# Performance work log

Measured on AMD Instinct MI355X. Metric: run time of the kernel, lower is better.

## Reference

```python
import jax, jax.numpy as jnp
import numpy as np

N_NODES = 50000


def _gcn_norm(edge_index, num_nodes):
    # Add self-loops (PyG GCNConv default, fill_value=1.0) and compute
    # symmetric normalization: norm_e = d^-1/2[row_e] * d^-1/2[col_e].
    loops = jnp.arange(num_nodes, dtype=edge_index.dtype)
    row = jnp.concatenate([edge_index[0], loops])
    col = jnp.concatenate([edge_index[1], loops])
    w = jnp.ones(row.shape[0], dtype=jnp.float32)
    deg = jax.ops.segment_sum(w, col, num_segments=num_nodes)
    dinv = jnp.where(deg > 0, jax.lax.rsqrt(deg), 0.0)
    norm = dinv[row] * w * dinv[col]
    return row, col, norm


def _gcn_conv(x, W, b, row, col, norm, num_nodes):
    h = x @ W                               # [N, out] dense GEMM
    msg = h[row] * norm[:, None]            # gather + scale  [E2, out]
    out = jax.ops.segment_sum(msg, col, num_segments=num_nodes)
    return out + b


def setup_inputs() -> dict:
    key = jax.random.key(0)
    k1, k2, k3, k4 = jax.random.split(key, 4)
    F, H, C, E = 512, 256, 64, 800000
    x = jax.random.normal(k1, (N_NODES, F), dtype=jnp.float32)
    edge_index = jax.random.randint(k2, (2, E), 0, N_NODES, dtype=jnp.int64)
    W1 = jax.random.normal(k3, (F, H), dtype=jnp.float32) * (1.0 / np.sqrt(F))
    b1 = jnp.zeros((H,), dtype=jnp.float32)
    W2 = jax.random.normal(k4, (H, C), dtype=jnp.float32) * (1.0 / np.sqrt(H))
    b2 = jnp.zeros((C,), dtype=jnp.float32)
    return {"x": x, "edge_index": edge_index, "W1": W1, "b1": b1, "W2": W2, "b2": b2}


def reference(x, edge_index, W1, b1, W2, b2):
    n = x.shape[0]
    row, col, norm = _gcn_norm(edge_index, n)
    h = _gcn_conv(x, W1, b1, row, col, norm, n)
    h = jax.nn.relu(h)                      # dropout is identity in eval
    out = _gcn_conv(h, W2, b2, row, col, norm, n)
    return out                              # do_omit_softmax=False -> Identity head
```

## Files before the change

kernel.cpp:

```cpp
#include <hip/hip_runtime.h>


typedef __bf16 bf16x8 __attribute__((ext_vector_type(8)));
typedef __bf16 bf16x4 __attribute__((ext_vector_type(4)));
typedef float  f32x4  __attribute__((ext_vector_type(4)));

#define N_NODES  50000
#define N_PAD    50048
#define ZERO_ROW 50000
#define F_IN     512
#define F_HID    256
#define F_OUT    64
#define SCAN_B   196

__global__ __launch_bounds__(256) void convw_kernel(
    const float* __restrict__ W, __bf16* __restrict__ WT, int K, int N)
{
    int i = blockIdx.x * blockDim.x + threadIdx.x;
    if (i >= N * K) return;
    int n = i / K, k = i - n * K;
    WT[i] = (__bf16)W[(size_t)k * N + n];
}

__global__ __launch_bounds__(256) void initsrc_kernel(
    int* __restrict__ srcidx, int n4)
{
    int i = blockIdx.x * blockDim.x + threadIdx.x;
    if (i < n4) {
        int4 v = make_int4(ZERO_ROW, ZERO_ROW, ZERO_ROW, ZERO_ROW);
        *(int4*)(srcidx + i * 4) = v;
    }
}

__global__ __launch_bounds__(256) void count_kernel(
    const int* __restrict__ col, int E, int Nn, int* __restrict__ cnt)
{
    int e0 = (blockIdx.x * blockDim.x + threadIdx.x) * 4;
    if (e0 >= E) return;
    int4 cc = *(const int4*)(col + e0);
    if ((unsigned)cc.x < (unsigned)Nn) atomicAdd(&cnt[cc.x], 1);
    if ((unsigned)cc.y < (unsigned)Nn) atomicAdd(&cnt[cc.y], 1);
    if ((unsigned)cc.z < (unsigned)Nn) atomicAdd(&cnt[cc.z], 1);
    if ((unsigned)cc.w < (unsigned)Nn) atomicAdd(&cnt[cc.w], 1);
}

__global__ __launch_bounds__(256) void scan_partial_kernel(
    const int* __restrict__ cnt, int* __restrict__ bsum, int N)
{
    __shared__ int s[256];
    const int t = threadIdx.x;
    const int i = blockIdx.x * 256 + t;
    int v = (i < N) ? ((cnt[i] + 1 + 7) & ~7) : 0;
    s[t] = v;
    __syncthreads();
    #pragma unroll
    for (int off = 128; off > 0; off >>= 1) {
        if (t < off) s[t] += s[t + off];
        __syncthreads();
    }
    if (t == 0) bsum[blockIdx.x] = s[0];
}

__global__ __launch_bounds__(256) void scan_bsum_kernel(
    const int* __restrict__ bsum, int* __restrict__ bofs,
    int* __restrict__ offs, int N, int PB)
{
    __shared__ int s[256];
    const int t = threadIdx.x;
    int v = (t < PB) ? bsum[t] : 0;
    s[t] = v;
    __syncthreads();
    #pragma unroll
    for (int off = 1; off < 256; off <<= 1) {
        int u = (t >= off) ? s[t - off] : 0;
        __syncthreads();
        s[t] += u;
        __syncthreads();
    }
    if (t < PB) bofs[t] = s[t] - v;
    if (t == 255) offs[N] = s[255];
}

__global__ __launch_bounds__(256) void scan_fill_kernel(
    const int* __restrict__ cnt, const int* __restrict__ bofs,
    int* __restrict__ offs, float* __restrict__ dinv, int N)
{
    __shared__ int s[256];
    const int t = threadIdx.x;
    const int i = blockIdx.x * 256 + t;
    int c   = (i < N) ? cnt[i] + 1 : 0;
    int cap = (c + 7) & ~7;
    s[t] = cap;
    __syncthreads();
    #pragma unroll
    for (int off = 1; off < 256; off <<= 1) {
        int u = (t >= off) ? s[t - off] : 0;
        __syncthreads();
        s[t] += u;
        __syncthreads();
    }
    if (i < N) {
        offs[i] = bofs[blockIdx.x] + s[t] - cap;
        dinv[i] = rsqrtf((float)c);
    }
}

__global__ __launch_bounds__(256) void fill_kernel(
    const int* __restrict__ row, const int* __restrict__ col,
    int E, int Nn, const int* __restrict__ offs,
    int* __restrict__ fill, int* __restrict__ srcidx)
{
    int e0 = (blockIdx.x * blockDim.x + threadIdx.x) * 4;
    int total = E + Nn;
    if (e0 >= total) return;
    int rr[4], cc[4];
    #pragma unroll
    for (int j = 0; j < 4; ++j) {
        int e = e0 + j;
        if (e < E)      { cc[j] = col[e]; rr[j] = row[e]; }
        else            { int i = e - E; cc[j] = (i < Nn) ? i : -1; rr[j] = cc[j]; }
    }
    #pragma unroll
    for (int j = 0; j < 4; ++j) {
        int c = cc[j], r = rr[j];
        if ((unsigned)c < (unsigned)Nn && (unsigned)r < (unsigned)Nn) {
            int p = offs[c] + atomicAdd(&fill[c], 1);
            srcidx[p] = r;
        }
    }
}

__global__ __launch_bounds__(256, 2) void gemm1_kernel(
    const float* __restrict__ A, const __bf16* __restrict__ BT,
    const float* __restrict__ dinv, __bf16* __restrict__ C)
{
    const int tid  = threadIdx.x;
    const int lane = tid & 63;
    const int wid  = tid >> 6;
    const int wm = wid >> 1, wn = wid & 1;
    const int bm = blockIdx.x * 64;
    const int lr = lane & 15, kg = lane >> 4;

    const int row0 = bm + wm * 32 + lr;
    const int row1 = row0 + 16;
    const int r0c = (row0 < N_NODES) ? row0 : 0;
    const int r1c = (row1 < N_NODES) ? row1 : 0;
    const float*  pa0 = A  + (size_t)r0c * F_IN + kg * 8;
    const float*  pa1 = A  + (size_t)r1c * F_IN + kg * 8;
    const __bf16* pb  = BT + (size_t)(wn * 128 + lr) * F_IN + kg * 8;

    float4 fa[4][2][2];
    bf16x8 fb[2][8];
    f32x4  acc[2][8] = {};

#define LA(i) {                                                    \
        fa[(i) & 3][0][0] = *(const float4*)(pa0 + (i) * 32);      \
        fa[(i) & 3][0][1] = *(const float4*)(pa0 + (i) * 32 + 4);  \
        fa[(i) & 3][1][0] = *(const float4*)(pa1 + (i) * 32);      \
        fa[(i) & 3][1][1] = *(const float4*)(pa1 + (i) * 32 + 4); }
#define LB(i) {                                                    \
        _Pragma("unroll")                                          \
        for (int n = 0; n < 8; ++n)                                \
            fb[(i) & 1][n] = *(const bf16x8*)(pb + (size_t)n * 16 * F_IN + (i) * 32); }

    LA(0) LA(1) LA(2)
    LB(0)

    #pragma unroll
    for (int kc = 0; kc < 16; ++kc) {
        if (kc + 3 < 16) LA(kc + 3)
        if (kc + 1 < 16) LB(kc + 1)
        bf16x8 wa[2];
        #pragma unroll
        for (int m = 0; m < 2; ++m) {
            float4 x0 = fa[kc & 3][m][0], x1 = fa[kc & 3][m][1];
            wa[m][0]=(__bf16)x0.x; wa[m][1]=(__bf16)x0.y;
            wa[m][2]=(__bf16)x0.z; wa[m][3]=(__bf16)x0.w;
            wa[m][4]=(__bf16)x1.x; wa[m][5]=(__bf16)x1.y;
            wa[m][6]=(__bf16)x1.z; wa[m][7]=(__bf16)x1.w;
        }
        #pragma unroll
        for (int m = 0; m < 2; ++m)
            #pragma unroll
            for (int n = 0; n < 8; ++n)
                acc[m][n] = __builtin_amdgcn_mfma_f32_16x16x32_bf16(
                    wa[m], fb[kc & 1][n], acc[m][n], 0, 0, 0);
    }
#undef LA
#undef LB

    const int crow0 = bm + wm * 32 + kg * 4;
    const int ccol0 = wn * 128 + lr;
    #pragma unroll
    for (int m = 0; m < 2; ++m) {
        #pragma unroll
        for (int j = 0; j < 4; ++j) {
            int r = crow0 + m * 16 + j;
            float dv = (r < N_NODES) ? dinv[r] : 0.f;
            #pragma unroll
            for (int n = 0; n < 8; ++n)
                C[(size_t)r * F_HID + (ccol0 + n * 16)] = (__bf16)(dv * acc[m][n][j]);
        }
    }
}

template<int WGM, int WGN, int FM, int FN>
__global__ __launch_bounds__(256) void gemm_kernel(
    const __bf16* __restrict__ A, const __bf16* __restrict__ BT,
    const float* __restrict__ dinv, __bf16* __restrict__ C, int K, int N)
{
    constexpr int BM = WGM * FM * 16;
    constexpr int BN = WGN * FN * 16;
    constexpr int BK = 32;
    constexpr int LDT = BK + 8;
    __shared__ __bf16 As[BM * LDT];
    __shared__ __bf16 Bs[BN * LDT];

    const int tid  = threadIdx.x;
    const int lane = tid & 63;
    const int wid  = tid >> 6;
    const int wm = wid / WGN, wn = wid % WGN;
    const int bm = blockIdx.x * BM;
    const int bn = blockIdx.y * BN;
    const int lr = lane & 15, kg = lane >> 4;

    const int arow = tid >> 2;
    const int achk = (tid & 3) * 8;

    f32x4 acc[FM][FN] = {};

    for (int k0 = 0; k0 < K; k0 += BK) {
        bf16x8 ra[BM / 64], rb[BN / 64];
        #pragma unroll
        for (int p = 0; p < BM / 64; ++p)
            ra[p] = *(const bf16x8*)(A + (size_t)(bm + p * 64 + arow) * K + k0 + achk);
        #pragma unroll
        for (int p = 0; p < BN / 64; ++p)
            rb[p] = *(const bf16x8*)(BT + (size_t)(bn + p * 64 + arow) * K + k0 + achk);
        __syncthreads();
        #pragma unroll
        for (int p = 0; p < BM / 64; ++p)
            *(bf16x8*)(As + (p * 64 + arow) * LDT + achk) = ra[p];
        #pragma unroll
        for (int p = 0; p < BN / 64; ++p)
            *(bf16x8*)(Bs + (p * 64 + arow) * LDT + achk) = rb[p];
        __syncthreads();

        bf16x8 af[FM], bfv[FN];
        #pragma unroll
        for (int m = 0; m < FM; ++m)
            af[m] = *(const bf16x8*)(As + (wm * FM * 16 + m * 16 + lr) * LDT + kg * 8);
        #pragma unroll
        for (int n = 0; n < FN; ++n)
            bfv[n] = *(const bf16x8*)(Bs + (wn * FN * 16 + n * 16 + lr) * LDT + kg * 8);
        #pragma unroll
        for (int m = 0; m < FM; ++m)
            #pragma unroll
            for (int n = 0; n < FN; ++n)
                acc[m][n] = __builtin_amdgcn_mfma_f32_16x16x32_bf16(
                    af[m], bfv[n], acc[m][n], 0, 0, 0);
    }

    const int crow0 = bm + wm * FM * 16 + kg * 4;
    const int ccol0 = bn + wn * FN * 16 + lr;
    #pragma unroll
    for (int m = 0; m < FM; ++m) {
        #pragma unroll
        for (int j = 0; j < 4; ++j) {
            int r = crow0 + m * 16 + j;
            float dv = (r < N_NODES) ? dinv[r] : 0.f;
            #pragma unroll
            for (int n = 0; n < FN; ++n)
                C[(size_t)r * N + (ccol0 + n * 16)] = (__bf16)(dv * acc[m][n][j]);
        }
    }
}

template<int F, int FP, bool RELU, bool BF16OUT>
__global__ __launch_bounds__(256) void agg_kernel(
    const __bf16* __restrict__ H,
    const int* __restrict__ offs, const int* __restrict__ srcidx,
    const float* __restrict__ dinv, const float* __restrict__ bias,
    __bf16* __restrict__ outb, float* __restrict__ outf,
    int Nn, int Mpad)
{
    const int lane = threadIdx.x & 63;
    const int node = blockIdx.x * 4 + (threadIdx.x >> 6);
    if (node >= Mpad) return;
    if (node >= Nn) {
        if (BF16OUT) {
            #pragma unroll
            for (int j = 0; j < FP; ++j)
                outb[(size_t)node * F + lane * FP + j] = (__bf16)0.f;
        }
        return;
    }
    const int e0 = offs[node], e1 = offs[node + 1];
    const float dv = dinv[node];
    float acc[FP] = {};
    for (int e = e0; e < e1; e += 8) {
        int4 sa = *(const int4*)(srcidx + e);
        int4 sb = *(const int4*)(srcidx + e + 4);
        if constexpr (FP == 4) {
            bf16x4 v0 = *(const bf16x4*)(H + (size_t)sa.x * F + lane * 4);
            bf16x4 v1 = *(const bf16x4*)(H + (size_t)sa.y * F + lane * 4);
            bf16x4 v2 = *(const bf16x4*)(H + (size_t)sa.z * F + lane * 4);
            bf16x4 v3 = *(const bf16x4*)(H + (size_t)sa.w * F + lane * 4);
            bf16x4 v4 = *(const bf16x4*)(H + (size_t)sb.x * F + lane * 4);
            bf16x4 v5 = *(const bf16x4*)(H + (size_t)sb.y * F + lane * 4);
            bf16x4 v6 = *(const bf16x4*)(H + (size_t)sb.z * F + lane * 4);
            bf16x4 v7 = *(const bf16x4*)(H + (size_t)sb.w * F + lane * 4);
            #pragma unroll
            for (int j = 0; j < 4; ++j)
                acc[j] += ((float)v0[j] + (float)v1[j] + (float)v2[j] + (float)v3[j])
                        + ((float)v4[j] + (float)v5[j] + (float)v6[j] + (float)v7[j]);
        } else {
            __bf16 v0 = H[(size_t)sa.x * F + lane];
            __bf16 v1 = H[(size_t)sa.y * F + lane];
            __bf16 v2 = H[(size_t)sa.z * F + lane];
            __bf16 v3 = H[(size_t)sa.w * F + lane];
            __bf16 v4 = H[(size_t)sb.x * F + lane];
            __bf16 v5 = H[(size_t)sb.y * F + lane];
            __bf16 v6 = H[(size_t)sb.z * F + lane];
            __bf16 v7 = H[(size_t)sb.w * F + lane];
            acc[0] += ((float)v0 + (float)v1 + (float)v2 + (float)v3)
                    + ((float)v4 + (float)v5 + (float)v6 + (float)v7);
        }
    }
    if constexpr (BF16OUT) {
        bf16x4 ov;
        #pragma unroll
        for (int j = 0; j < FP; ++j) {
            float r = dv * acc[j] + bias[lane * FP + j];
            if (RELU) r = fmaxf(r, 0.f);
            if constexpr (FP == 4) ov[j] = (__bf16)r;
            else outb[(size_t)node * F + lane] = (__bf16)r;
        }
        if constexpr (FP == 4)
            *(bf16x4*)(outb + (size_t)node * F + lane * 4) = ov;
    } else {
        #pragma unroll
        for (int j = 0; j < FP; ++j) {
            float r = dv * acc[j] + bias[lane * FP + j];
            if (RELU) r = fmaxf(r, 0.f);
            outf[(size_t)node * F + lane * FP + j] = r;
        }
    }
}

extern "C" void kernel_launch(void* const* d_in, const int* in_sizes, int n_in,
                              void* d_out, int out_size, void* d_ws, size_t ws_size,
                              hipStream_t stream)
{
    const float* x   = (const float*)d_in[0];
    const int*   ei  = (const int*)d_in[1];
    const float* W1  = (const float*)d_in[2];
    const float* b1  = (const float*)d_in[3];
    const float* W2  = (const float*)d_in[4];
    const float* b2  = (const float*)d_in[5];
    const int E  = in_sizes[1] / 2;
    const int Nn = N_NODES;
    const int E2P = E + 8 * Nn;
    const int* rowp = ei;
    const int* colp = ei + E;

    char* w = (char*)d_ws;
    auto alloc = [&](size_t bytes) {
        char* p = w; w += (bytes + 255) & ~(size_t)255; return p;
    };
    __bf16* h1   = (__bf16*)alloc((size_t)N_PAD * F_HID * 2);
    __bf16* h2   = (__bf16*)alloc((size_t)N_PAD * F_HID * 2);
    __bf16* w1t  = (__bf16*)alloc((size_t)F_HID * F_IN  * 2);
    __bf16* w2t  = (__bf16*)alloc((size_t)F_OUT * F_HID * 2);
    int*    cnt  = (int*)  alloc((size_t)Nn * 4);
    int*    fil  = (int*)  alloc((size_t)Nn * 4);
    int*    offs = (int*)  alloc((size_t)(Nn + 1) * 4);
    float*  dinv = (float*)alloc((size_t)Nn * 4);
    int*    bsum = (int*)  alloc((size_t)SCAN_B * 4);
    int*    bofs = (int*)  alloc((size_t)SCAN_B * 4);
    int*    srcx = (int*)  alloc((size_t)E2P * 4);
    __bf16* t2 = h1;

    hipMemsetAsync(cnt, 0, (size_t)Nn * 4, stream);
    hipMemsetAsync(fil, 0, (size_t)Nn * 4, stream);
    initsrc_kernel<<<(E2P / 4 + 255) / 256, 256, 0, stream>>>(srcx, E2P / 4);

    convw_kernel<<<(F_IN * F_HID + 255) / 256, 256, 0, stream>>>(W1, w1t, F_IN, F_HID);
    convw_kernel<<<(F_HID * F_OUT + 255) / 256, 256, 0, stream>>>(W2, w2t, F_HID, F_OUT);

    count_kernel<<<(E / 4 + 255) / 256, 256, 0, stream>>>(colp, E, Nn, cnt);
    scan_partial_kernel<<<SCAN_B, 256, 0, stream>>>(cnt, bsum, Nn);
    scan_bsum_kernel<<<1, 256, 0, stream>>>(bsum, bofs, offs, Nn, SCAN_B);
    scan_fill_kernel<<<SCAN_B, 256, 0, stream>>>(cnt, bofs, offs, dinv, Nn);
    fill_kernel<<<((E + Nn) / 4 + 255) / 256, 256, 0, stream>>>(
        rowp, colp, E, Nn, offs, fil, srcx);

    gemm1_kernel<<<N_PAD / 64, 256, 0, stream>>>(x, w1t, dinv, h1);
    agg_kernel<F_HID, 4, true, true><<<N_PAD / 4, 256, 0, stream>>>(
        h1, offs, srcx, dinv, b1, h2, nullptr, Nn, N_PAD);

    gemm_kernel<4, 1, 1, 4><<<dim3(N_PAD / 64, 1), 256, 0, stream>>>(
        h2, w2t, dinv, t2, F_HID, F_OUT);
    agg_kernel<F_OUT, 1, false, false><<<(Nn + 3) / 4, 256, 0, stream>>>(
        t2, offs, srcx, dinv, b2, nullptr, (float*)d_out, Nn, Nn);
}
```

Measured before the change: 431.5 us.

## Stage gemm1 tiles through LDS with direct global-to-LDS loads and swizzle

Replaces gemm1's per-wave register prefetching of A and B fragments with a shared LDS tile per block, filled by global_load_lds instructions and read back through an XOR swizzle to avoid bank conflicts. Waves now share the B tile instead of each loading its own copy from global memory, and the occupancy hint is raised from 2 to 4 blocks. The cost is that the loop is no longer software-pipelined: two barriers per k-step and no double buffering, so load latency is exposed unless the extra occupancy hides it.

```diff
diff --git a/kernel.cpp b/kernel.cpp
--- a/kernel.cpp
+++ b/kernel.cpp
@@ -13,6 +13,10 @@
 #define F_OUT    64
 #define SCAN_B   196
 
+#define GLOAD_LDS16(gp, lp) __builtin_amdgcn_global_load_lds(               \
+    (const __attribute__((address_space(1))) void*)(gp),                    \
+    (__attribute__((address_space(3))) void*)(lp), 16, 0, 0)
+
 __global__ __launch_bounds__(256) void convw_kernel(
     const float* __restrict__ W, __bf16* __restrict__ WT, int K, int N)
 {
@@ -130,64 +134,76 @@
     }
 }
 
-__global__ __launch_bounds__(256, 2) void gemm1_kernel(
+__global__ __launch_bounds__(256, 4) void gemm1_kernel(
     const float* __restrict__ A, const __bf16* __restrict__ BT,
     const float* __restrict__ dinv, __bf16* __restrict__ C)
 {
+    __shared__ __align__(16) unsigned char lds[24576];
+
     const int tid  = threadIdx.x;
     const int lane = tid & 63;
-    const int wid  = tid >> 6;
-    const int wm = wid >> 1, wn = wid & 1;
+    const int wv   = tid >> 6;
+    const int wm = wv >> 1, wn = wv & 1;
     const int bm = blockIdx.x * 64;
     const int lr = lane & 15, kg = lane >> 4;
 
-    const int row0 = bm + wm * 32 + lr;
-    const int row1 = row0 + 16;
-    const int r0c = (row0 < N_NODES) ? row0 : 0;
-    const int r1c = (row1 < N_NODES) ? row1 : 0;
-    const float*  pa0 = A  + (size_t)r0c * F_IN + kg * 8;
-    const float*  pa1 = A  + (size_t)r1c * F_IN + kg * 8;
-    const __bf16* pb  = BT + (size_t)(wn * 128 + lr) * F_IN + kg * 8;
-
-    float4 fa[4][2][2];
-    bf16x8 fb[2][8];
-    f32x4  acc[2][8] = {};
-
-#define LA(i) {                                                    \
-        fa[(i) & 3][0][0] = *(const float4*)(pa0 + (i) * 32);      \
-        fa[(i) & 3][0][1] = *(const float4*)(pa0 + (i) * 32 + 4);  \
-        fa[(i) & 3][1][0] = *(const float4*)(pa1 + (i) * 32);      \
-        fa[(i) & 3][1][1] = *(const float4*)(pa1 + (i) * 32 + 4); }
-#define LB(i) {                                                    \
-        _Pragma("unroll")                                          \
-        for (int n = 0; n < 8; ++n)                                \
-            fb[(i) & 1][n] = *(const bf16x8*)(pb + (size_t)n * 16 * F_IN + (i) * 32); }
-
-    LA(0) LA(1) LA(2)
-    LB(0)
-
-    #pragma unroll
-    for (int kc = 0; kc < 16; ++kc) {
-        if (kc + 3 < 16) LA(kc + 3)
-        if (kc + 1 < 16) LB(kc + 1)
-        bf16x8 wa[2];
+    const int cA = (lane & 7) ^ (lane >> 3);
+    const int cB = (lane & 3) ^ ((lane >> 3) & 3);
+
+    int arowA[2]; const float* gA[2]; unsigned char* lA[2];
+    #pragma unroll
+    for (int q = 0; q < 2; ++q) {
+        int s   = wv * 2 + q;
+        int row = s * 8 + (lane >> 3);
+        int gr  = bm + row;
+        if (gr >= N_NODES) gr = 0;
+        arowA[q] = row;
+        gA[q] = A + (size_t)gr * F_IN + cA * 4;
+        lA[q] = lds + s * 1024;
+    }
+    const __bf16* gB[4]; unsigned char* lB[4];
+    #pragma unroll
+    for (int q = 0; q < 4; ++q) {
+        int s   = wv * 4 + q;
+        int row = s * 16 + (lane >> 2);
+        gB[q] = BT + (size_t)row * F_IN + cB * 8;
+        lB[q] = lds + 8192 + s * 1024;
+    }
+
+    f32x4 acc[2][8] = {};
+
+    for (int k0 = 0; k0 < F_IN; k0 += 32) {
+        __syncthreads();
+        #pragma unroll
+        for (int q = 0; q < 2; ++q) GLOAD_LDS16(gA[q] + k0, lA[q]);
+        #pragma unroll
+        for (int q = 0; q < 4; ++q) GLOAD_LDS16(gB[q] + k0, lB[q]);
+        __syncthreads();
+
+        bf16x8 af[2];
         #pragma unroll
         for (int m = 0; m < 2; ++m) {
-            float4 x0 = fa[kc & 3][m][0], x1 = fa[kc & 3][m][1];
-            wa[m][0]=(__bf16)x0.x; wa[m][1]=(__bf16)x0.y;
-            wa[m][2]=(__bf16)x0.z; wa[m][3]=(__bf16)x0.w;
-            wa[m][4]=(__bf16)x1.x; wa[m][5]=(__bf16)x1.y;
-            wa[m][6]=(__bf16)x1.z; wa[m][7]=(__bf16)x1.w;
-        }
-        #pragma unroll
-        for (int m = 0; m < 2; ++m)
-            #pragma unroll
-            for (int n = 0; n < 8; ++n)
+            int ar = wm * 32 + m * 16 + lr;
+            int h0 = ((kg << 1)     ) ^ (ar & 7);
+            int h1 = ((kg << 1) | 1 ) ^ (ar & 7);
+            float4 x0 = *(const float4*)(lds + (ar << 7) + (h0 << 4));
+            float4 x1 = *(const float4*)(lds + (ar << 7) + (h1 << 4));
+            af[m][0]=(__bf16)x0.x; af[m][1]=(__bf16)x0.y;
+            af[m][2]=(__bf16)x0.z; af[m][3]=(__bf16)x0.w;
+            af[m][4]=(__bf16)x1.x; af[m][5]=(__bf16)x1.y;
+            af[m][6]=(__bf16)x1.z; af[m][7]=(__bf16)x1.w;
+        }
+        #pragma unroll
+        for (int n = 0; n < 8; ++n) {
+            int br = wn * 128 + n * 16 + lr;
+            int ph = kg ^ ((br >> 1) & 3);
+            bf16x8 bf = *(const bf16x8*)(lds + 8192 + (br << 6) + (ph << 4));
+            #pragma unroll
+            for (int m = 0; m < 2; ++m)
                 acc[m][n] = __builtin_amdgcn_mfma_f32_16x16x32_bf16(
-                    wa[m], fb[kc & 1][n], acc[m][n], 0, 0, 0);
-    }
-#undef LA
-#undef LB
+                    af[m], bf, acc[m][n], 0, 0, 0);
+        }
+    }
 
     const int crow0 = bm + wm * 32 + kg * 4;
     const int ccol0 = wn * 128 + lr;
```

After: 374.4 us. 1.15x faster.
